# Kernel tuning notes

Hardware: AMD Instinct MI355X
Metric: run time of the kernel (lower is better)

Reference implementation:

```python
import jax, jax.numpy as jnp
import numpy as np
from jax.scipy.special import logsumexp

TEMPERATURE = 0.1
BETA = 0.999
EPS = 1e-8
HARD_K = 10  # min(num_classes // 4, 10) with num_classes = 1000


def _l2norm(x, axis=-1):
    return x * jax.lax.rsqrt(jnp.sum(x * x, axis=axis, keepdims=True) + 1e-24)


def setup_inputs() -> dict:
    key = jax.random.key(0)
    k1, k2, k3, k4, k5 = jax.random.split(key, 5)
    B, D, C, M = 4096, 1024, 1000, 32768
    return {
        "image_features": jax.random.normal(k1, (B, D), dtype=jnp.float32),
        "prompts": jax.random.normal(k2, (C, D), dtype=jnp.float32),
        "labels": jax.random.randint(k3, (B, C), 0, 2, dtype=jnp.int32),
        "memory_features": jax.random.normal(k4, (M, D), dtype=jnp.float32),
        "memory_labels": jax.random.randint(k5, (M, C), 0, 2, dtype=jnp.int32),
        "mem_ptr": 16384,
    }


def reference(image_features, prompts, labels, memory_features, memory_labels, mem_ptr):
    B, D = image_features.shape
    C = prompts.shape[0]
    labels_f = labels.astype(jnp.float32)

    # z_img = F.normalize(image_features)
    z_img = _l2norm(image_features, axis=1)

    # class weights (effective-number reweighting), computed from this batch's labels
    counts = labels_f.sum(axis=0)                              # [C]
    effective_num = 1.0 - jnp.power(jnp.float32(BETA), counts)
    weights = (1.0 - BETA) / (effective_num + EPS)
    weights = weights / jnp.sum(weights) * C                   # [C]

    # memory bank update (detached write of current batch at ptr), then use [:ptr+B]
    mem_f = memory_features.at[mem_ptr:mem_ptr + B].set(jax.lax.stop_gradient(z_img))
    mem_l = memory_labels.at[mem_ptr:mem_ptr + B].set(labels)
    used = mem_ptr + B  # static

    enhanced_features = jnp.concatenate([z_img, mem_f[:used]], axis=0)     # [N, D]
    enhanced_labels = jnp.concatenate([labels_f, mem_l[:used].astype(jnp.float32)], axis=0)  # [N, C]

    z_prompts = _l2norm(prompts, axis=1)                       # [C, D]
    sim = (enhanced_features @ z_prompts.T) / TEMPERATURE      # [N, C]

    pos_mask = enhanced_labels > 0                             # [N, C]

    # hard negatives: top-K similarities among negatives define the keep threshold
    sim_for_neg = jnp.where(pos_mask, -jnp.inf, sim)
    hard_neg_vals, _ = jax.lax.top_k(sim_for_neg, HARD_K)      # [N, K]
    min_hard_neg = hard_neg_vals[:, -1:]                       # [N, 1]
    neg_mask = (~pos_mask) & (sim >= min_hard_neg)
    full_mask = pos_mask | neg_mask

    lse = logsumexp(jnp.where(full_mask, sim, -jnp.inf), axis=1)  # [N]
    log_prob = sim - lse[:, None]                              # [N, C]

    posf = pos_mask.astype(sim.dtype)
    pos_w = posf * weights[None, :]                            # [N, C]
    weight_sums = pos_w.sum(axis=1)                            # [N]
    loss_num = (pos_w * (-log_prob)).sum(axis=1)               # [N]

    valid = weight_sums > 0
    loss_per_sample = jnp.where(valid, loss_num / (weight_sums + EPS), 0.0)
    n_valid = jnp.maximum(valid.sum(), 1)
    attr_loss = loss_per_sample.sum() / n_valid.astype(sim.dtype)
    # single attribute -> total_loss / num_valid_attrs == attr_loss
    return attr_loss
```

## Files before the change

### kernel.cpp

```cpp
#include <hip/hip_runtime.h>
#include <math.h>

#define BN    4096
#define DD    1024
#define CC    1000
#define MM    32768
#define ROWS_CAP 32768
#define SIMLD 1024

typedef __attribute__((ext_vector_type(8))) short short8;
typedef __attribute__((ext_vector_type(4))) short short4v;
typedef __attribute__((ext_vector_type(4))) float f32x4;

__device__ __forceinline__ float wave_max_f(float v) {
#pragma unroll
  for (int off = 32; off >= 1; off >>= 1) v = fmaxf(v, __shfl_xor(v, off, 64));
  return v;
}
__device__ __forceinline__ float wave_sum_f(float v) {
#pragma unroll
  for (int off = 32; off >= 1; off >>= 1) v += __shfl_xor(v, off, 64);
  return v;
}

__device__ __forceinline__ short f2bf(float f) {
  union { float f; unsigned u; } v; v.f = f;
  unsigned r = v.u + 0x7FFF + ((v.u >> 16) & 1);
  return (short)(r >> 16);
}
__device__ __forceinline__ float bf2f(unsigned short u) {
  union { unsigned u; float f; } v; v.u = ((unsigned)u) << 16;
  return v.f;
}

__device__ __forceinline__ void gload16(const short* g, short* l) {
  __builtin_amdgcn_global_load_lds(
      (const __attribute__((address_space(1))) unsigned int*)g,
      (__attribute__((address_space(3))) unsigned int*)l, 16, 0, 0);
}

__global__ __launch_bounds__(256) void count_kernel(const int* __restrict__ labels,
                                                    int* __restrict__ counts) {
  const int c = blockIdx.x * 256 + threadIdx.x;
  if (c >= CC) return;
  const int b0 = blockIdx.y * 64;
  int s = 0;
  for (int b = b0; b < b0 + 64; ++b) s += labels[(size_t)b * CC + c];
  atomicAdd(&counts[c], s);
}

__global__ __launch_bounds__(1024) void weights_kernel(const int* __restrict__ counts,
                                                       float* __restrict__ weights) {
  const int t = threadIdx.x;
  float w = 0.f;
  if (t < CC) {
    float cnt = (float)counts[t];
    float en = 1.0f - expf(cnt * logf(0.999f));
    w = (1.0f - 0.999f) / (en + 1e-8f);
  }
  float s = wave_sum_f(w);
  __shared__ float part[16];
  if ((t & 63) == 0) part[t >> 6] = s;
  __syncthreads();
  float tot = 0.f;
#pragma unroll
  for (int i = 0; i < 16; ++i) tot += part[i];
  if (t < CC) weights[t] = w * ((float)CC / tot);
}

__global__ __launch_bounds__(256) void convB_kernel(const float* __restrict__ prompts,
                                                    short* __restrict__ B) {
  const int row = blockIdx.x;
  const int t = threadIdx.x;
  short4v o = {0, 0, 0, 0};
  if (row < CC) {
    float4 v = ((const float4*)(prompts + (size_t)row * DD))[t];
    float s = v.x * v.x + v.y * v.y + v.z * v.z + v.w * v.w;
    s = wave_sum_f(s);
    __shared__ float part[4];
    if ((t & 63) == 0) part[t >> 6] = s;
    __syncthreads();
    float sc = 10.0f * rsqrtf(part[0] + part[1] + part[2] + part[3] + 1e-24f);
    o[0] = f2bf(v.x * sc); o[1] = f2bf(v.y * sc);
    o[2] = f2bf(v.z * sc); o[3] = f2bf(v.w * sc);
  }
  ((short4v*)(B + (size_t)row * DD))[t] = o;
}

__global__ __launch_bounds__(256) void convA_kernel(const float* __restrict__ img,
                                                    const float* __restrict__ mem,
                                                    const int* __restrict__ memptr,
                                                    short* __restrict__ A) {
  const int nrows = BN + memptr[0];
  const int padded = (nrows + 127) & ~127;
  const int row = blockIdx.x;
  if (row >= padded) return;
  const int t = threadIdx.x;
  short4v o = {0, 0, 0, 0};
  if (row < nrows) {
    const float* src = (row < BN) ? img + (size_t)row * DD
                                  : mem + (size_t)(row - BN) * DD;
    float4 v = ((const float4*)src)[t];
    float sc = 1.0f;
    if (row < BN) {
      float s = v.x * v.x + v.y * v.y + v.z * v.z + v.w * v.w;
      s = wave_sum_f(s);
      __shared__ float part[4];
      if ((t & 63) == 0) part[t >> 6] = s;
      __syncthreads();
      sc = rsqrtf(part[0] + part[1] + part[2] + part[3] + 1e-24f);
    }
    o[0] = f2bf(v.x * sc); o[1] = f2bf(v.y * sc);
    o[2] = f2bf(v.z * sc); o[3] = f2bf(v.w * sc);
  }
  ((short4v*)(A + (size_t)row * DD))[t] = o;
}

__global__ __launch_bounds__(256) void gemm_mfma(const short* __restrict__ A,
                                                 const short* __restrict__ Bm,
                                                 const int* __restrict__ memptr,
                                                 short* __restrict__ simbf, int lo) {
  const int nrows = BN + memptr[0];
  const int row0 = blockIdx.y * 128;
  if (lo + row0 >= nrows) return;
  const int c0 = blockIdx.x * 128;

  __shared__ short As[128 * 32];
  __shared__ short Bs[128 * 32];

  const int t = threadIdx.x;
  const int lane = t & 63;
  const int wid = t >> 6;
  const int wm = (wid >> 1) * 64;
  const int wn = (wid & 1) * 64;

  const short* ga0 = A + (size_t)(row0 + (t >> 2)) * DD + (t & 3) * 8;
  const short* ga1 = ga0 + (size_t)64 * DD;
  const short* gb0 = Bm + (size_t)(c0 + (t >> 2)) * DD + (t & 3) * 8;
  const short* gb1 = gb0 + (size_t)64 * DD;
  short* lA0 = As + t * 8;
  short* lA1 = As + 2048 + t * 8;
  short* lB0 = Bs + t * 8;
  short* lB1 = Bs + 2048 + t * 8;

  f32x4 acc[4][4] = {};
  const int ka = (lane >> 4) * 8;
  const int lm = lane & 15;

  for (int k0 = 0; k0 < DD; k0 += 32) {
    gload16(ga0, lA0); gload16(ga1, lA1);
    gload16(gb0, lB0); gload16(gb1, lB1);
    ga0 += 32; ga1 += 32; gb0 += 32; gb1 += 32;
    __syncthreads();
    short8 af[4], bfr[4];
#pragma unroll
    for (int i = 0; i < 4; ++i)
      af[i] = *(const short8*)(As + (wm + i * 16 + lm) * 32 + ka);
#pragma unroll
    for (int i = 0; i < 4; ++i)
      bfr[i] = *(const short8*)(Bs + (wn + i * 16 + lm) * 32 + ka);
#pragma unroll
    for (int mi = 0; mi < 4; ++mi)
#pragma unroll
      for (int ni = 0; ni < 4; ++ni)
        acc[mi][ni] = __builtin_amdgcn_mfma_f32_16x16x32_bf16(af[mi], bfr[ni], acc[mi][ni], 0, 0, 0);
    __syncthreads();
  }

  const int rbase = row0 + wm + (lane >> 4) * 4;
#pragma unroll
  for (int ni = 0; ni < 4; ++ni) {
    const int col = c0 + wn + ni * 16 + lm;
#pragma unroll
    for (int mi = 0; mi < 4; ++mi) {
      f32x4 v = acc[mi][ni];
      const int rl = rbase + mi * 16;
#pragma unroll
      for (int r = 0; r < 4; ++r)
        simbf[(size_t)(rl + r) * SIMLD + col] = f2bf(v[r]);
    }
  }
}

__global__ __launch_bounds__(256) void rowpost_kernel(
    const short* __restrict__ simbf, const int* __restrict__ labels,
    const int* __restrict__ mlabels, const float* __restrict__ weights,
    const int* __restrict__ memptr, float* __restrict__ lps_arr,
    float* __restrict__ valid_arr, int chunk_lo) {
  __shared__ float wlds[1024];
  {
    const int t = threadIdx.x;
#pragma unroll
    for (int i = 0; i < 4; ++i) {
      int c = t + i * 256;
      wlds[c] = (c < CC) ? weights[c] : 0.f;
    }
  }
  __syncthreads();

  const int nrows = BN + memptr[0];
  const int wid = threadIdx.x >> 6;
  const int lane = threadIdx.x & 63;
  const int row = chunk_lo + blockIdx.x * 4 + wid;
  if (row >= ROWS_CAP) return;
  if (row >= nrows) {
    if (lane == 0) { lps_arr[row] = 0.f; valid_arr[row] = 0.f; }
    return;
  }

  const unsigned short* srow = (const unsigned short*)simbf + (size_t)(row - chunk_lo) * SIMLD;
  const int* lrow = (row < BN) ? labels + (size_t)row * CC
                               : mlabels + (size_t)(row - BN) * CC;
  float sv[16];
  bool pv[16];
  float vneg[16];
#pragma unroll
  for (int j = 0; j < 16; ++j) {
    int c = lane + 64 * j;
    bool ok = (c < CC);
    float s = ok ? bf2f(srow[c]) : -INFINITY;
    bool p = ok && (lrow[c] > 0);
    sv[j] = ok ? s : -INFINITY;
    pv[j] = p;
    vneg[j] = (ok && !p) ? s : -INFINITY;
  }

  float v10 = -INFINITY;
  for (int r = 0; r < 10; ++r) {
    float lmx = -INFINITY;
#pragma unroll
    for (int j = 0; j < 16; ++j) lmx = fmaxf(lmx, vneg[j]);
    lmx = wave_max_f(lmx);
#pragma unroll
    for (int j = 0; j < 16; ++j) if (vneg[j] == lmx) vneg[j] = -INFINITY;
    v10 = lmx;
  }

  float mmax = -INFINITY;
#pragma unroll
  for (int j = 0; j < 16; ++j) {
    if (pv[j] || sv[j] >= v10) mmax = fmaxf(mmax, sv[j]);
  }
  mmax = wave_max_f(mmax);

  float esum = 0.f, wsum = 0.f, wsim = 0.f;
#pragma unroll
  for (int j = 0; j < 16; ++j) {
    int c = lane + 64 * j;
    if (c < CC) {
      if (pv[j] || sv[j] >= v10) esum += expf(sv[j] - mmax);
      if (pv[j]) { float w = wlds[c]; wsum += w; wsim += w * sv[j]; }
    }
  }
  esum = wave_sum_f(esum);
  wsum = wave_sum_f(wsum);
  wsim = wave_sum_f(wsim);

  if (lane == 0) {
    float lse = mmax + logf(esum);
    bool valid = (wsum > 0.f);
    float lps = valid ? (wsum * lse - wsim) / (wsum + 1e-8f) : 0.f;
    float mult = (row < BN) ? 2.f : 1.f;
    lps_arr[row] = mult * lps;
    valid_arr[row] = valid ? mult : 0.f;
  }
}

__global__ __launch_bounds__(1024) void reduce_kernel(const float* __restrict__ lps_arr,
                                                      const float* __restrict__ valid_arr,
                                                      float* __restrict__ out) {
  const int t = threadIdx.x;
  float s1 = 0.f, s2 = 0.f;
  for (int i = t; i < ROWS_CAP; i += 1024) { s1 += lps_arr[i]; s2 += valid_arr[i]; }
  s1 = wave_sum_f(s1);
  s2 = wave_sum_f(s2);
  __shared__ float p1[16], p2[16];
  if ((t & 63) == 0) { p1[t >> 6] = s1; p2[t >> 6] = s2; }
  __syncthreads();
  if (t == 0) {
    float a = 0.f, b = 0.f;
#pragma unroll
    for (int i = 0; i < 16; ++i) { a += p1[i]; b += p2[i]; }
    out[0] = a / fmaxf(b, 1.0f);
  }
}

extern "C" void kernel_launch(void* const* d_in, const int* in_sizes, int n_in,
                              void* d_out, int out_size, void* d_ws, size_t ws_size,
                              hipStream_t stream) {
  const float* img     = (const float*)d_in[0];
  const float* prompts = (const float*)d_in[1];
  const int*   labels  = (const int*)d_in[2];
  const float* mem     = (const float*)d_in[3];
  const int*   mlabels = (const int*)d_in[4];
  const int*   memptr  = (const int*)d_in[5];
  float* out = (float*)d_out;
  char* ws = (char*)d_ws;

  int*   counts  = (int*)(ws + 0);
  float* weights = (float*)(ws + 4096);
  float* lps_arr = (float*)(ws + 8192);
  float* val_arr = (float*)(ws + 139264);
  short* Bbf     = (short*)(ws + 270336);
  const size_t fixed = 2367488;

  long long avail = (long long)ws_size - (long long)fixed;
  int chunk = (int)(avail / 4096);
  chunk &= ~127;
  if (chunk < 128) chunk = 128;
  if (chunk > ROWS_CAP) chunk = ROWS_CAP;
  short* Abf   = (short*)(ws + fixed);
  short* simbf = (short*)(ws + fixed + (size_t)chunk * 2048);

  hipMemsetAsync(ws, 0, 4096, stream);

  count_kernel<<<dim3((CC + 255) / 256, BN / 64), 256, 0, stream>>>(labels, counts);
  weights_kernel<<<1, 1024, 0, stream>>>(counts, weights);
  convB_kernel<<<1024, 256, 0, stream>>>(prompts, Bbf);

  for (int lo = 0; lo < ROWS_CAP; lo += chunk) {
    int rows = (ROWS_CAP - lo < chunk) ? (ROWS_CAP - lo) : chunk;
    if (lo == 0 || lo < ROWS_CAP) {
    }
    convA_kernel<<<rows, 256, 0, stream>>>(img, mem, memptr, Abf - (size_t)lo * 0 + 0);
    dim3 g(1024 / 128, rows / 128);
    gemm_mfma<<<g, 256, 0, stream>>>(Abf, Bbf, memptr, simbf, lo);
    rowpost_kernel<<<rows / 4, 256, 0, stream>>>(simbf, labels, mlabels, weights, memptr,
                                                 lps_arr, val_arr, lo);
  }
  reduce_kernel<<<1, 1024, 0, stream>>>(lps_arr, val_arr, out);
}
```

Measured before the change: 371.1 us.

## Fuse conversion kernels, widen GEMM K-tile with swizzled LDS, remap block order

Merges the prompt and feature bf16 conversion kernels into one launch that converts all rows once, into a full-size A buffer instead of per-chunk conversion. The GEMM now stages 64-wide K tiles with an XOR-swizzled LDS layout to avoid bank conflicts and halve barrier count, and uses a 1D grid remapped so groups of row tiles share column tiles for L2 reuse. The final reduction is vectorised with float4 loads. The full A buffer raises workspace needs, and the chunk size is now rounded to 1024 rows.

```diff
diff --git a/kernel.cpp b/kernel.cpp
--- a/kernel.cpp
+++ b/kernel.cpp
@@ -68,34 +68,35 @@
   if (t < CC) weights[t] = w * ((float)CC / tot);
 }
 
-__global__ __launch_bounds__(256) void convB_kernel(const float* __restrict__ prompts,
-                                                    short* __restrict__ B) {
-  const int row = blockIdx.x;
+__global__ __launch_bounds__(256) void conv_kernel(const float* __restrict__ img,
+                                                   const float* __restrict__ prompts,
+                                                   const float* __restrict__ mem,
+                                                   const int* __restrict__ memptr,
+                                                   short* __restrict__ A,
+                                                   short* __restrict__ B) {
+  __shared__ float part[4];
   const int t = threadIdx.x;
-  short4v o = {0, 0, 0, 0};
-  if (row < CC) {
-    float4 v = ((const float4*)(prompts + (size_t)row * DD))[t];
-    float s = v.x * v.x + v.y * v.y + v.z * v.z + v.w * v.w;
-    s = wave_sum_f(s);
-    __shared__ float part[4];
-    if ((t & 63) == 0) part[t >> 6] = s;
-    __syncthreads();
-    float sc = 10.0f * rsqrtf(part[0] + part[1] + part[2] + part[3] + 1e-24f);
-    o[0] = f2bf(v.x * sc); o[1] = f2bf(v.y * sc);
-    o[2] = f2bf(v.z * sc); o[3] = f2bf(v.w * sc);
-  }
-  ((short4v*)(B + (size_t)row * DD))[t] = o;
-}
-
-__global__ __launch_bounds__(256) void convA_kernel(const float* __restrict__ img,
-                                                    const float* __restrict__ mem,
-                                                    const int* __restrict__ memptr,
-                                                    short* __restrict__ A) {
+  const int blk = blockIdx.x;
+  if (blk >= ROWS_CAP) {
+    const int row = blk - ROWS_CAP;
+    short4v o = {0, 0, 0, 0};
+    if (row < CC) {
+      float4 v = ((const float4*)(prompts + (size_t)row * DD))[t];
+      float s = v.x * v.x + v.y * v.y + v.z * v.z + v.w * v.w;
+      s = wave_sum_f(s);
+      if ((t & 63) == 0) part[t >> 6] = s;
+      __syncthreads();
+      float sc = 10.0f * rsqrtf(part[0] + part[1] + part[2] + part[3] + 1e-24f);
+      o[0] = f2bf(v.x * sc); o[1] = f2bf(v.y * sc);
+      o[2] = f2bf(v.z * sc); o[3] = f2bf(v.w * sc);
+    }
+    ((short4v*)(B + (size_t)row * DD))[t] = o;
+    return;
+  }
   const int nrows = BN + memptr[0];
   const int padded = (nrows + 127) & ~127;
-  const int row = blockIdx.x;
+  const int row = blk;
   if (row >= padded) return;
-  const int t = threadIdx.x;
   short4v o = {0, 0, 0, 0};
   if (row < nrows) {
     const float* src = (row < BN) ? img + (size_t)row * DD
@@ -105,7 +106,6 @@
     if (row < BN) {
       float s = v.x * v.x + v.y * v.y + v.z * v.z + v.w * v.w;
       s = wave_sum_f(s);
-      __shared__ float part[4];
       if ((t & 63) == 0) part[t >> 6] = s;
       __syncthreads();
       sc = rsqrtf(part[0] + part[1] + part[2] + part[3] + 1e-24f);
@@ -120,13 +120,19 @@
                                                  const short* __restrict__ Bm,
                                                  const int* __restrict__ memptr,
                                                  short* __restrict__ simbf, int lo) {
+  const int f = blockIdx.x;
+  const int x = f & 7;
+  const int s = f >> 3;
+  const int c = s & 7;
+  const int rt = (s >> 3) * 8 + x;
+
   const int nrows = BN + memptr[0];
-  const int row0 = blockIdx.y * 128;
+  const int row0 = rt * 128;
   if (lo + row0 >= nrows) return;
-  const int c0 = blockIdx.x * 128;
-
-  __shared__ short As[128 * 32];
-  __shared__ short Bs[128 * 32];
+  const int c0 = c * 128;
+
+  __shared__ short As[128 * 64];
+  __shared__ short Bs[128 * 64];
 
   const int t = threadIdx.x;
   const int lane = t & 63;
@@ -134,36 +140,43 @@
   const int wm = (wid >> 1) * 64;
   const int wn = (wid & 1) * 64;
 
-  const short* ga0 = A + (size_t)(row0 + (t >> 2)) * DD + (t & 3) * 8;
-  const short* ga1 = ga0 + (size_t)64 * DD;
-  const short* gb0 = Bm + (size_t)(c0 + (t >> 2)) * DD + (t & 3) * 8;
-  const short* gb1 = gb0 + (size_t)64 * DD;
-  short* lA0 = As + t * 8;
-  short* lA1 = As + 2048 + t * 8;
-  short* lB0 = Bs + t * 8;
-  short* lB1 = Bs + 2048 + t * 8;
+  const int srow = t >> 3;
+  const int gchunk = (t & 7) ^ (srow & 7);
+  const short* ga = A + (size_t)(lo + row0 + srow) * DD + gchunk * 8;
+  const short* gb = Bm + (size_t)(c0 + srow) * DD + gchunk * 8;
+  short* lA = As + t * 8;
+  short* lB = Bs + t * 8;
 
   f32x4 acc[4][4] = {};
-  const int ka = (lane >> 4) * 8;
   const int lm = lane & 15;
-
-  for (int k0 = 0; k0 < DD; k0 += 32) {
-    gload16(ga0, lA0); gload16(ga1, lA1);
-    gload16(gb0, lB0); gload16(gb1, lB1);
-    ga0 += 32; ga1 += 32; gb0 += 32; gb1 += 32;
+  const int q0 = lane >> 4;
+
+  for (int k0 = 0; k0 < DD; k0 += 64) {
+#pragma unroll
+    for (int p = 0; p < 4; ++p) gload16(ga + (size_t)(p * 32) * DD + k0, lA + p * 2048);
+#pragma unroll
+    for (int p = 0; p < 4; ++p) gload16(gb + (size_t)(p * 32) * DD + k0, lB + p * 2048);
     __syncthreads();
-    short8 af[4], bfr[4];
-#pragma unroll
-    for (int i = 0; i < 4; ++i)
-      af[i] = *(const short8*)(As + (wm + i * 16 + lm) * 32 + ka);
-#pragma unroll
-    for (int i = 0; i < 4; ++i)
-      bfr[i] = *(const short8*)(Bs + (wn + i * 16 + lm) * 32 + ka);
-#pragma unroll
-    for (int mi = 0; mi < 4; ++mi)
-#pragma unroll
-      for (int ni = 0; ni < 4; ++ni)
-        acc[mi][ni] = __builtin_amdgcn_mfma_f32_16x16x32_bf16(af[mi], bfr[ni], acc[mi][ni], 0, 0, 0);
+#pragma unroll
+    for (int kk = 0; kk < 2; ++kk) {
+      short8 af[4], bfr[4];
+      const int qc = q0 + kk * 4;
+#pragma unroll
+      for (int i = 0; i < 4; ++i) {
+        int m = wm + i * 16 + lm;
+        af[i] = *(const short8*)(As + m * 64 + ((qc ^ (m & 7)) * 8));
+      }
+#pragma unroll
+      for (int i = 0; i < 4; ++i) {
+        int n = wn + i * 16 + lm;
+        bfr[i] = *(const short8*)(Bs + n * 64 + ((qc ^ (n & 7)) * 8));
+      }
+#pragma unroll
+      for (int mi = 0; mi < 4; ++mi)
+#pragma unroll
+        for (int ni = 0; ni < 4; ++ni)
+          acc[mi][ni] = __builtin_amdgcn_mfma_f32_16x16x32_bf16(af[mi], bfr[ni], acc[mi][ni], 0, 0, 0);
+    }
     __syncthreads();
   }
 
@@ -270,8 +283,16 @@
                                                       const float* __restrict__ valid_arr,
                                                       float* __restrict__ out) {
   const int t = threadIdx.x;
+  const float4* l4 = (const float4*)lps_arr;
+  const float4* v4 = (const float4*)valid_arr;
   float s1 = 0.f, s2 = 0.f;
-  for (int i = t; i < ROWS_CAP; i += 1024) { s1 += lps_arr[i]; s2 += valid_arr[i]; }
+#pragma unroll
+  for (int i = 0; i < 8; ++i) {
+    float4 a = l4[t + i * 1024];
+    float4 b = v4[t + i * 1024];
+    s1 += a.x + a.y + a.z + a.w;
+    s2 += b.x + b.y + b.z + b.w;
+  }
   s1 = wave_sum_f(s1);
   s2 = wave_sum_f(s2);
   __shared__ float p1[16], p2[16];
@@ -302,29 +323,26 @@
   float* lps_arr = (float*)(ws + 8192);
   float* val_arr = (float*)(ws + 139264);
   short* Bbf     = (short*)(ws + 270336);
-  const size_t fixed = 2367488;
+  short* Abf     = (short*)(ws + 2367488);
+  const size_t fixed = 2367488 + (size_t)ROWS_CAP * DD * 2;
+  short* simbf   = (short*)(ws + fixed);
 
   long long avail = (long long)ws_size - (long long)fixed;
-  int chunk = (int)(avail / 4096);
-  chunk &= ~127;
-  if (chunk < 128) chunk = 128;
+  int chunk = (int)(avail / (SIMLD * 2));
+  chunk &= ~1023;
+  if (chunk < 1024) chunk = 1024;
   if (chunk > ROWS_CAP) chunk = ROWS_CAP;
-  short* Abf   = (short*)(ws + fixed);
-  short* simbf = (short*)(ws + fixed + (size_t)chunk * 2048);
 
   hipMemsetAsync(ws, 0, 4096, stream);
 
+  conv_kernel<<<ROWS_CAP + 1024, 256, 0, stream>>>(img, prompts, mem, memptr, Abf, Bbf);
   count_kernel<<<dim3((CC + 255) / 256, BN / 64), 256, 0, stream>>>(labels, counts);
   weights_kernel<<<1, 1024, 0, stream>>>(counts, weights);
-  convB_kernel<<<1024, 256, 0, stream>>>(prompts, Bbf);
 
   for (int lo = 0; lo < ROWS_CAP; lo += chunk) {
     int rows = (ROWS_CAP - lo < chunk) ? (ROWS_CAP - lo) : chunk;
-    if (lo == 0 || lo < ROWS_CAP) {
-    }
-    convA_kernel<<<rows, 256, 0, stream>>>(img, mem, memptr, Abf - (size_t)lo * 0 + 0);
-    dim3 g(1024 / 128, rows / 128);
-    gemm_mfma<<<g, 256, 0, stream>>>(Abf, Bbf, memptr, simbf, lo);
+    int rowTiles = rows / 128;
+    gemm_mfma<<<8 * rowTiles, 256, 0, stream>>>(Abf, Bbf, memptr, simbf, lo);
     rowpost_kernel<<<rows / 4, 256, 0, stream>>>(simbf, labels, mlabels, weights, memptr,
                                                  lps_arr, val_arr, lo);
   }
```

Result: faster. 355.5 us (-4.2%).
